# Kernel tuning notes

Hardware: AMD Instinct MI355X
Metric: run time of the kernel (lower is better)

Reference implementation:

```python
import jax, jax.numpy as jnp
import numpy as np

B, N, F_IN, F_OUT = 8, 2048, 128, 128


def setup_inputs() -> dict:
    key = jax.random.key(0)
    k1, k2, k3, k4 = jax.random.split(key, 4)
    stdv = 1.0 / np.sqrt(F_OUT)
    X = jax.random.normal(k1, (B, N, F_IN), dtype=jnp.float32)
    adj = jax.random.uniform(k2, (B, N, N), dtype=jnp.float32)
    W = jax.random.uniform(k3, (F_IN, F_OUT), minval=-stdv, maxval=stdv, dtype=jnp.float32)
    b = jax.random.uniform(k4, (F_OUT,), minval=-stdv, maxval=stdv, dtype=jnp.float32)
    return {"X": X, "adj": adj, "W": W, "b": b}


def reference(X, adj, W, b):
    # XW: [B, N, F_out]
    XW = jnp.einsum('bnf,fo->bno', X, W)
    # adj + I (self loops)
    adj = adj + jnp.eye(adj.shape[1], dtype=adj.dtype)[None]
    # symmetric degree normalization: D^-1/2 A D^-1/2, done as row/col scaling
    d = jnp.sum(adj, axis=-1)                 # [B, N]
    r = d ** -0.5                             # [B, N]
    adj = adj * r[:, :, None] * r[:, None, :] # [B, N, N]
    y = jnp.einsum('bnm,bmo->bno', adj, XW) + b
    return jax.nn.leaky_relu(y, negative_slope=0.01)
```

## Files before the change

kernel.cpp:

```cpp
#include <hip/hip_runtime.h>
#include <hip/hip_bf16.h>

#define BB 8
#define NN 2048
#define FD 128

typedef float f32x4 __attribute__((ext_vector_type(4)));
typedef short bf16x8 __attribute__((ext_vector_type(8)));
typedef short s16x4 __attribute__((ext_vector_type(4)));

__device__ __forceinline__ short f2bf(float f) {
  union { __hip_bfloat16 h; short s; } u;
  u.h = __float2bfloat16(f);
  return u.s;
}

__global__ __launch_bounds__(256) void k_degree(const float* __restrict__ adj,
                                                float* __restrict__ r) {
  const int row  = blockIdx.x * 4 + (threadIdx.x >> 6);
  const int lane = threadIdx.x & 63;
  const f32x4* p = reinterpret_cast<const f32x4*>(adj + (size_t)row * NN);
  float s = 0.f;
#pragma unroll
  for (int i = 0; i < 8; ++i) {
    f32x4 v = p[lane + 64 * i];
    s += (v.x + v.y) + (v.z + v.w);
  }
#pragma unroll
  for (int off = 32; off >= 1; off >>= 1) s += __shfl_xor(s, off, 64);
  if (lane == 0) r[row] = rsqrtf(1.0f + s);
}

__global__ __launch_bounds__(256) void k_xw(const float* __restrict__ X,
                                            const float* __restrict__ W,
                                            const float* __restrict__ r,
                                            short* __restrict__ bpack,
                                            float* __restrict__ xwsr) {
  __shared__ __align__(16) float Xs[64][132];
  __shared__ __align__(16) float Ws[128][128];
  const int b  = blockIdx.y;
  const int m0 = blockIdx.x * 64;
  const int t  = threadIdx.x;
  {
    const f32x4* wp = reinterpret_cast<const f32x4*>(W);
    f32x4* wd = reinterpret_cast<f32x4*>(&Ws[0][0]);
#pragma unroll
    for (int i = 0; i < 16; ++i) wd[t + 256 * i] = wp[t + 256 * i];
    const f32x4* xp = reinterpret_cast<const f32x4*>(X + ((size_t)b * NN + m0) * FD);
#pragma unroll
    for (int i = 0; i < 8; ++i) {
      int slot = t + 256 * i;
      f32x4 v = xp[slot];
      *reinterpret_cast<f32x4*>(&Xs[slot >> 5][(slot & 31) * 4]) = v;
    }
  }
  __syncthreads();
  const int ot = (t & 15) * 8;
  const int mt = (t >> 4) * 4;
  float acc[4][8];
#pragma unroll
  for (int i = 0; i < 4; ++i)
#pragma unroll
    for (int j = 0; j < 8; ++j) acc[i][j] = 0.f;

  for (int k = 0; k < 128; k += 4) {
    f32x4 xv[4];
#pragma unroll
    for (int i = 0; i < 4; ++i) xv[i] = *reinterpret_cast<const f32x4*>(&Xs[mt + i][k]);
#pragma unroll
    for (int kk = 0; kk < 4; ++kk) {
      float wv[8];
#pragma unroll
      for (int j = 0; j < 8; ++j) wv[j] = Ws[k + kk][ot + j];
#pragma unroll
      for (int i = 0; i < 4; ++i)
#pragma unroll
        for (int j = 0; j < 8; ++j) acc[i][j] = fmaf(xv[i][kk], wv[j], acc[i][j]);
    }
  }
  const int bm = b * NN + m0 + mt;
#pragma unroll
  for (int i = 0; i < 4; ++i) {
    float rm = r[bm + i];
#pragma unroll
    for (int j = 0; j < 8; ++j) acc[i][j] *= rm;
  }
#pragma unroll
  for (int i = 0; i < 4; ++i) {
    f32x4 lo = {acc[i][0], acc[i][1], acc[i][2], acc[i][3]};
    f32x4 hi = {acc[i][4], acc[i][5], acc[i][6], acc[i][7]};
    float* dst = xwsr + (size_t)(bm + i) * FD + ot;
    *reinterpret_cast<f32x4*>(dst) = lo;
    *reinterpret_cast<f32x4*>(dst + 4) = hi;
  }
  short* bp = bpack + (size_t)b * NN * FD;
  const int grp = (m0 + mt) >> 3;
  const int h   = ((m0 + mt) >> 2) & 1;
#pragma unroll
  for (int j = 0; j < 8; ++j) {
    s16x4 sv;
#pragma unroll
    for (int i = 0; i < 4; ++i) sv[i] = f2bf(acc[i][j]);
    *reinterpret_cast<s16x4*>(bp + (size_t)grp * 1024 + (ot + j) * 8 + h * 4) = sv;
  }
}

__global__ __launch_bounds__(256) void k_gemm(const float* __restrict__ adj,
                                              const short* __restrict__ bpack,
                                              const float* __restrict__ xwsr,
                                              const float* __restrict__ r,
                                              const float* __restrict__ bias,
                                              float* __restrict__ out) {
  __shared__ __align__(16) short As[2][64 * 64];
  const int b    = blockIdx.y;
  const int n0   = blockIdx.x * 64;
  const int t    = threadIdx.x;
  const int lane = t & 63;
  const int w    = t >> 6;
  const float* adjb = adj + (size_t)b * NN * NN;
  const short* bp   = bpack + (size_t)b * NN * FD;

  f32x4 zero = {0.f, 0.f, 0.f, 0.f};
  f32x4 acc[4][2];
#pragma unroll
  for (int i = 0; i < 4; ++i)
#pragma unroll
    for (int j = 0; j < 2; ++j) acc[i][j] = zero;

  auto stage_load = [&](int k0, f32x4 (&v)[4]) {
#pragma unroll
    for (int i = 0; i < 4; ++i) {
      int slot = t + 256 * i;
      v[i] = *reinterpret_cast<const f32x4*>(adjb + (size_t)(n0 + (slot >> 4)) * NN + k0 + (slot & 15) * 4);
    }
  };
  auto stage_write = [&](int buf, f32x4 (&v)[4]) {
#pragma unroll
    for (int i = 0; i < 4; ++i) {
      int slot = t + 256 * i;
      int rr = slot >> 4, c4 = slot & 15;
      s16x4 sv;
      sv[0] = f2bf(v[i][0]); sv[1] = f2bf(v[i][1]);
      sv[2] = f2bf(v[i][2]); sv[3] = f2bf(v[i][3]);
      int off = rr * 128 + ((c4 * 8) ^ ((rr & 7) << 4));
      *reinterpret_cast<s16x4*>(reinterpret_cast<char*>(&As[buf][0]) + off) = sv;
    }
  };
  auto load_bfrag = [&](int k0, bf16x8 (&bf)[2][2]) {
    const int ob = w * 32 + (lane & 15);
    const int kb = (k0 >> 3) + (lane >> 4);
#pragma unroll
    for (int kk = 0; kk < 2; ++kk)
#pragma unroll
      for (int of = 0; of < 2; ++of)
        bf[kk][of] = *reinterpret_cast<const bf16x8*>(bp + (size_t)(kb + kk * 4) * 1024 + (ob + of * 16) * 8);
  };

  f32x4 nx[4];
  bf16x8 bcur[2][2], bnext[2][2];
  stage_load(0, nx);
  stage_write(0, nx);
  load_bfrag(0, bcur);
  __syncthreads();

  for (int tile = 0; tile < 32; ++tile) {
    if (tile < 31) {
      stage_load((tile + 1) * 64, nx);
      load_bfrag((tile + 1) * 64, bnext);
    }
    const char* abase = reinterpret_cast<const char*>(&As[tile & 1][0]);
#pragma unroll
    for (int kk = 0; kk < 2; ++kk) {
      bf16x8 af[4];
#pragma unroll
      for (int rg = 0; rg < 4; ++rg) {
        int rr = rg * 16 + (lane & 15);
        int off = rr * 128 + (((kk * 32 + (lane >> 4) * 8) * 2) ^ ((rr & 7) << 4));
        af[rg] = *reinterpret_cast<const bf16x8*>(abase + off);
      }
#pragma unroll
      for (int rg = 0; rg < 4; ++rg)
#pragma unroll
        for (int of = 0; of < 2; ++of)
          acc[rg][of] = __builtin_amdgcn_mfma_f32_16x16x32_bf16(af[rg], bcur[kk][of], acc[rg][of], 0, 0, 0);
    }
    if (tile < 31) {
      stage_write((tile + 1) & 1, nx);
#pragma unroll
      for (int kk = 0; kk < 2; ++kk)
#pragma unroll
        for (int of = 0; of < 2; ++of) bcur[kk][of] = bnext[kk][of];
    }
    __syncthreads();
  }

  const int col = lane & 15, rq = lane >> 4;
#pragma unroll
  for (int rg = 0; rg < 4; ++rg) {
#pragma unroll
    for (int reg = 0; reg < 4; ++reg) {
      const int n = n0 + rg * 16 + rq * 4 + reg;
      const float rn = r[b * NN + n];
      const size_t rowb = ((size_t)b * NN + n) * FD;
#pragma unroll
      for (int of = 0; of < 2; ++of) {
        const int o = w * 32 + of * 16 + col;
        float v = acc[rg][of][reg] + xwsr[rowb + o];
        v = rn * v + bias[o];
        out[rowb + o] = v > 0.f ? v : 0.01f * v;
      }
    }
  }
}

extern "C" void kernel_launch(void* const* d_in, const int* in_sizes, int n_in,
                              void* d_out, int out_size, void* d_ws, size_t ws_size,
                              hipStream_t stream) {
  (void)in_sizes; (void)n_in; (void)out_size; (void)ws_size;
  const float* X    = (const float*)d_in[0];
  const float* adj  = (const float*)d_in[1];
  const float* W    = (const float*)d_in[2];
  const float* bias = (const float*)d_in[3];
  float* out = (float*)d_out;

  char* ws = (char*)d_ws;
  float* r     = (float*)ws;
  short* bpack = (short*)(ws + 65536);
  float* xwsr  = (float*)(ws + 65536 + (size_t)BB * NN * FD * 2);

  k_degree<<<dim3(BB * NN / 4), dim3(256), 0, stream>>>(adj, r);
  k_xw<<<dim3(NN / 64, BB), dim3(256), 0, stream>>>(X, W, r, bpack, xwsr);
  k_gemm<<<dim3(NN / 64, BB), dim3(256), 0, stream>>>(adj, bpack, xwsr, r, bias, out);
}
```

Measured before the change: 74.96 us.

## Fuse degree reduction into XW kernel and drop LDS staging in adjacency GEMM

Folds the row-degree reduction into the XW kernel, so each block sums the adj rows it owns and keeps the rsqrt scales in shared memory. That removes one kernel launch. The adjacency GEMM is rewritten so each wave loads its own A rows straight from global memory into registers, converts them to bf16 in registers, and loads B fragments directly. Each wave covers all 128 output columns for 16 rows, with two-deep register double buffering and no LDS or barriers. The trade-offs: the fused kernel now has only 256 blocks to stream all of adj serially, each wave reads 32-byte strided chunks of adj, and each wave re-reads the full B slice from global memory.

```diff
diff --git a/kernel.cpp b/kernel.cpp
--- a/kernel.cpp
+++ b/kernel.cpp
@@ -15,32 +15,40 @@
   return u.s;
 }
 
-__global__ __launch_bounds__(256) void k_degree(const float* __restrict__ adj,
-                                                float* __restrict__ r) {
-  const int row  = blockIdx.x * 4 + (threadIdx.x >> 6);
-  const int lane = threadIdx.x & 63;
-  const f32x4* p = reinterpret_cast<const f32x4*>(adj + (size_t)row * NN);
-  float s = 0.f;
-#pragma unroll
-  for (int i = 0; i < 8; ++i) {
-    f32x4 v = p[lane + 64 * i];
-    s += (v.x + v.y) + (v.z + v.w);
-  }
-#pragma unroll
-  for (int off = 32; off >= 1; off >>= 1) s += __shfl_xor(s, off, 64);
-  if (lane == 0) r[row] = rsqrtf(1.0f + s);
-}
-
-__global__ __launch_bounds__(256) void k_xw(const float* __restrict__ X,
-                                            const float* __restrict__ W,
-                                            const float* __restrict__ r,
-                                            short* __restrict__ bpack,
-                                            float* __restrict__ xwsr) {
+__global__ __launch_bounds__(256) void k_xw_fused(const float* __restrict__ X,
+                                                  const float* __restrict__ adj,
+                                                  const float* __restrict__ W,
+                                                  short* __restrict__ bpack,
+                                                  float* __restrict__ xwsr,
+                                                  float* __restrict__ r) {
   __shared__ __align__(16) float Xs[64][132];
   __shared__ __align__(16) float Ws[128][128];
-  const int b  = blockIdx.y;
-  const int m0 = blockIdx.x * 64;
-  const int t  = threadIdx.x;
+  __shared__ float Ls[64];
+  const int b    = blockIdx.y;
+  const int m0   = blockIdx.x * 64;
+  const int t    = threadIdx.x;
+  const int lane = t & 63;
+  const int w    = t >> 6;
+
+  {
+    const float* base = adj + ((size_t)b * NN + m0 + w * 16) * NN;
+    for (int rr = 0; rr < 16; ++rr) {
+      const f32x4* p = reinterpret_cast<const f32x4*>(base + (size_t)rr * NN);
+      float s = 0.f;
+#pragma unroll
+      for (int i = 0; i < 8; ++i) {
+        f32x4 v = p[lane + 64 * i];
+        s += (v.x + v.y) + (v.z + v.w);
+      }
+#pragma unroll
+      for (int off = 32; off >= 1; off >>= 1) s += __shfl_xor(s, off, 64);
+      if (lane == 0) {
+        float rv = rsqrtf(1.0f + s);
+        Ls[w * 16 + rr] = rv;
+        r[b * NN + m0 + w * 16 + rr] = rv;
+      }
+    }
+  }
   {
     const f32x4* wp = reinterpret_cast<const f32x4*>(W);
     f32x4* wd = reinterpret_cast<f32x4*>(&Ws[0][0]);
@@ -55,6 +63,7 @@
     }
   }
   __syncthreads();
+
   const int ot = (t & 15) * 8;
   const int mt = (t >> 4) * 4;
   float acc[4][8];
@@ -81,7 +90,7 @@
   const int bm = b * NN + m0 + mt;
 #pragma unroll
   for (int i = 0; i < 4; ++i) {
-    float rm = r[bm + i];
+    float rm = Ls[mt + i];
 #pragma unroll
     for (int j = 0; j < 8; ++j) acc[i][j] *= rm;
   }
@@ -105,110 +114,70 @@
   }
 }
 
-__global__ __launch_bounds__(256) void k_gemm(const float* __restrict__ adj,
-                                              const short* __restrict__ bpack,
-                                              const float* __restrict__ xwsr,
-                                              const float* __restrict__ r,
-                                              const float* __restrict__ bias,
-                                              float* __restrict__ out) {
-  __shared__ __align__(16) short As[2][64 * 64];
+__global__ __launch_bounds__(256) void k_gemm2(const float* __restrict__ adj,
+                                               const short* __restrict__ bpack,
+                                               const float* __restrict__ xwsr,
+                                               const float* __restrict__ r,
+                                               const float* __restrict__ bias,
+                                               float* __restrict__ out) {
   const int b    = blockIdx.y;
   const int n0   = blockIdx.x * 64;
   const int t    = threadIdx.x;
   const int lane = t & 63;
   const int w    = t >> 6;
-  const float* adjb = adj + (size_t)b * NN * NN;
-  const short* bp   = bpack + (size_t)b * NN * FD;
-
-  f32x4 zero = {0.f, 0.f, 0.f, 0.f};
-  f32x4 acc[4][2];
-#pragma unroll
-  for (int i = 0; i < 4; ++i)
-#pragma unroll
-    for (int j = 0; j < 2; ++j) acc[i][j] = zero;
-
-  auto stage_load = [&](int k0, f32x4 (&v)[4]) {
-#pragma unroll
-    for (int i = 0; i < 4; ++i) {
-      int slot = t + 256 * i;
-      v[i] = *reinterpret_cast<const f32x4*>(adjb + (size_t)(n0 + (slot >> 4)) * NN + k0 + (slot & 15) * 4);
-    }
+  const int rowloc = w * 16 + (lane & 15);
+  const float* ap  = adj + ((size_t)b * NN + n0 + rowloc) * NN + (lane >> 4) * 8;
+  const short* bpb = bpack + (size_t)b * NN * FD + (size_t)(lane >> 4) * 1024 + (lane & 15) * 8;
+
+  f32x4 acc[8];
+#pragma unroll
+  for (int i = 0; i < 8; ++i) acc[i] = (f32x4){0.f, 0.f, 0.f, 0.f};
+
+  f32x4 aA[2], aB[2];
+  bf16x8 bA[8], bB[8];
+
+  auto loadA = [&](int ks, f32x4 (&d)[2]) {
+    const f32x4* p = reinterpret_cast<const f32x4*>(ap + ks * 32);
+    d[0] = p[0];
+    d[1] = p[1];
   };
-  auto stage_write = [&](int buf, f32x4 (&v)[4]) {
-#pragma unroll
-    for (int i = 0; i < 4; ++i) {
-      int slot = t + 256 * i;
-      int rr = slot >> 4, c4 = slot & 15;
-      s16x4 sv;
-      sv[0] = f2bf(v[i][0]); sv[1] = f2bf(v[i][1]);
-      sv[2] = f2bf(v[i][2]); sv[3] = f2bf(v[i][3]);
-      int off = rr * 128 + ((c4 * 8) ^ ((rr & 7) << 4));
-      *reinterpret_cast<s16x4*>(reinterpret_cast<char*>(&As[buf][0]) + off) = sv;
-    }
+  auto loadB = [&](int ks, bf16x8 (&d)[8]) {
+    const short* p = bpb + (size_t)ks * 4096;
+#pragma unroll
+    for (int ct = 0; ct < 8; ++ct)
+      d[ct] = *reinterpret_cast<const bf16x8*>(p + ct * 128);
   };
-  auto load_bfrag = [&](int k0, bf16x8 (&bf)[2][2]) {
-    const int ob = w * 32 + (lane & 15);
-    const int kb = (k0 >> 3) + (lane >> 4);
-#pragma unroll
-    for (int kk = 0; kk < 2; ++kk)
-#pragma unroll
-      for (int of = 0; of < 2; ++of)
-        bf[kk][of] = *reinterpret_cast<const bf16x8*>(bp + (size_t)(kb + kk * 4) * 1024 + (ob + of * 16) * 8);
+  auto step = [&](f32x4 (&sa)[2], bf16x8 (&sb)[8]) {
+    bf16x8 af;
+#pragma unroll
+    for (int i = 0; i < 4; ++i) { af[i] = f2bf(sa[0][i]); af[4 + i] = f2bf(sa[1][i]); }
+#pragma unroll
+    for (int ct = 0; ct < 8; ++ct)
+      acc[ct] = __builtin_amdgcn_mfma_f32_16x16x32_bf16(af, sb[ct], acc[ct], 0, 0, 0);
   };
 
-  f32x4 nx[4];
-  bf16x8 bcur[2][2], bnext[2][2];
-  stage_load(0, nx);
-  stage_write(0, nx);
-  load_bfrag(0, bcur);
-  __syncthreads();
-
-  for (int tile = 0; tile < 32; ++tile) {
-    if (tile < 31) {
-      stage_load((tile + 1) * 64, nx);
-      load_bfrag((tile + 1) * 64, bnext);
-    }
-    const char* abase = reinterpret_cast<const char*>(&As[tile & 1][0]);
-#pragma unroll
-    for (int kk = 0; kk < 2; ++kk) {
-      bf16x8 af[4];
-#pragma unroll
-      for (int rg = 0; rg < 4; ++rg) {
-        int rr = rg * 16 + (lane & 15);
-        int off = rr * 128 + (((kk * 32 + (lane >> 4) * 8) * 2) ^ ((rr & 7) << 4));
-        af[rg] = *reinterpret_cast<const bf16x8*>(abase + off);
-      }
-#pragma unroll
-      for (int rg = 0; rg < 4; ++rg)
-#pragma unroll
-        for (int of = 0; of < 2; ++of)
-          acc[rg][of] = __builtin_amdgcn_mfma_f32_16x16x32_bf16(af[rg], bcur[kk][of], acc[rg][of], 0, 0, 0);
-    }
-    if (tile < 31) {
-      stage_write((tile + 1) & 1, nx);
-#pragma unroll
-      for (int kk = 0; kk < 2; ++kk)
-#pragma unroll
-        for (int of = 0; of < 2; ++of) bcur[kk][of] = bnext[kk][of];
-    }
-    __syncthreads();
+  loadA(0, aA); loadB(0, bA);
+  loadA(1, aB); loadB(1, bB);
+  for (int ks = 0; ks < 64; ks += 2) {
+    step(aA, bA);
+    if (ks + 2 < 64) { loadA(ks + 2, aA); loadB(ks + 2, bA); }
+    step(aB, bB);
+    if (ks + 3 < 64) { loadA(ks + 3, aB); loadB(ks + 3, bB); }
   }
 
   const int col = lane & 15, rq = lane >> 4;
-#pragma unroll
-  for (int rg = 0; rg < 4; ++rg) {
-#pragma unroll
-    for (int reg = 0; reg < 4; ++reg) {
-      const int n = n0 + rg * 16 + rq * 4 + reg;
-      const float rn = r[b * NN + n];
-      const size_t rowb = ((size_t)b * NN + n) * FD;
-#pragma unroll
-      for (int of = 0; of < 2; ++of) {
-        const int o = w * 32 + of * 16 + col;
-        float v = acc[rg][of][reg] + xwsr[rowb + o];
-        v = rn * v + bias[o];
-        out[rowb + o] = v > 0.f ? v : 0.01f * v;
-      }
+  const float* xr = xwsr + ((size_t)b * NN + n0 + w * 16) * FD;
+  float* ob = out + ((size_t)b * NN + n0 + w * 16) * FD;
+#pragma unroll
+  for (int reg = 0; reg < 4; ++reg) {
+    const int rloc = rq * 4 + reg;
+    const float rn = r[b * NN + n0 + w * 16 + rloc];
+#pragma unroll
+    for (int ct = 0; ct < 8; ++ct) {
+      const int o = ct * 16 + col;
+      float v = acc[ct][reg] + xr[(size_t)rloc * FD + o];
+      v = rn * v + bias[o];
+      ob[(size_t)rloc * FD + o] = v > 0.f ? v : 0.01f * v;
     }
   }
 }
@@ -228,7 +197,6 @@
   short* bpack = (short*)(ws + 65536);
   float* xwsr  = (float*)(ws + 65536 + (size_t)BB * NN * FD * 2);
 
-  k_degree<<<dim3(BB * NN / 4), dim3(256), 0, stream>>>(adj, r);
-  k_xw<<<dim3(NN / 64, BB), dim3(256), 0, stream>>>(X, W, r, bpack, xwsr);
-  k_gemm<<<dim3(NN / 64, BB), dim3(256), 0, stream>>>(adj, bpack, xwsr, r, bias, out);
-}
+  k_xw_fused<<<dim3(NN / 64, BB), dim3(256), 0, stream>>>(X, adj, W, bpack, xwsr, r);
+  k_gemm2<<<dim3(NN / 64, BB), dim3(256), 0, stream>>>(adj, bpack, xwsr, r, bias, out);
+}
```

Measured after the change: 72.12 us. 1.04x faster.
